# Performance work log

Hardware: AMD Instinct MI355X
Metric: run time of the kernel (lower is better)

Reference implementation:

```python
import jax, jax.numpy as jnp
import numpy as np

H, NH, L, S, B, V = 512, 8, 6, 2048, 2, 32000
DH = H // NH
EPS = 1e-5


def posenc(h, s):
    pos = jnp.arange(s, dtype=jnp.float32)[:, None]
    div = jnp.power(10000.0, jnp.arange(0, h, 2, dtype=jnp.float32) / h)
    pe = jnp.zeros((s, h), dtype=jnp.float32)
    pe = pe.at[:, 0::2].set(jnp.sin(pos / div))
    pe = pe.at[:, 1::2].set(jnp.cos(pos / div))
    return pe


def layernorm(x, g, b):
    mu = jnp.mean(x, axis=-1, keepdims=True)
    var = jnp.mean(jnp.square(x - mu), axis=-1, keepdims=True)
    return (x - mu) * jax.lax.rsqrt(var + EPS) * g + b


def setup_inputs() -> dict:
    key = jax.random.key(0)
    ks = jax.random.split(key, 16)
    sc = 0.02
    return {
        "src": jax.random.randint(ks[0], (B, S), 0, V),
        "mask": jnp.ones((B, 1, 1, S), dtype=jnp.int32),
        "emb": jax.random.normal(ks[1], (V, H), jnp.float32) * sc,
        "Wq": jax.random.normal(ks[2], (L, H, H), jnp.float32) * sc,
        "bq": jnp.zeros((L, H), jnp.float32),
        "Wk": jax.random.normal(ks[3], (L, H, H), jnp.float32) * sc,
        "bk": jnp.zeros((L, H), jnp.float32),
        "Wv": jax.random.normal(ks[4], (L, H, H), jnp.float32) * sc,
        "bv": jnp.zeros((L, H), jnp.float32),
        "Wo": jax.random.normal(ks[5], (L, H, H), jnp.float32) * sc,
        "bo": jnp.zeros((L, H), jnp.float32),
        "gamma": jnp.ones((L, H), jnp.float32),
        "beta": jnp.zeros((L, H), jnp.float32),
        "W1": jax.random.normal(ks[6], (L, H, 4 * H), jnp.float32) * sc,
        "b1": jnp.zeros((L, 4 * H), jnp.float32),
        "W2": jax.random.normal(ks[7], (L, 4 * H, H), jnp.float32) * sc,
        "b2": jnp.zeros((L, H), jnp.float32),
    }


def reference(src, mask, emb, Wq, bq, Wk, bk, Wv, bv, Wo, bo, gamma, beta, W1, b1, W2, b2):
    x = emb[src] + posenc(H, S)[None, :, :]  # [B,S,H]
    for i in range(L):
        q = (x @ Wq[i] + bq[i]).reshape(B, S, NH, DH).transpose(0, 2, 1, 3)
        k = (x @ Wk[i] + bk[i]).reshape(B, S, NH, DH).transpose(0, 2, 1, 3)
        v = (x @ Wv[i] + bv[i]).reshape(B, S, NH, DH).transpose(0, 2, 1, 3)
        scores = jnp.einsum("bhqd,bhkd->bhqk", q, k) / jnp.sqrt(jnp.float32(DH))
        scores = jnp.where(mask == 0, jnp.float32(-1e20), scores)
        attn = jax.nn.softmax(scores, axis=-1)
        av = jnp.einsum("bhqk,bhkd->bhqd", attn, v)
        attn_out = av.transpose(0, 2, 1, 3).reshape(B, S, H) @ Wo[i] + bo[i]
        # NOTE: same LayerNorm params applied to both sublayers (as in source)
        res = x + layernorm(attn_out, gamma[i], beta[i])
        ffn = jax.nn.relu(res @ W1[i] + b1[i]) @ W2[i] + b2[i]
        x = res + layernorm(ffn, gamma[i], beta[i])
    return x
```

## Files before the change

kernel.cpp:

```cpp
#include <hip/hip_runtime.h>
#include <math.h>

#define HDIM 512
#define NHEAD 8
#define NLAYER 6
#define SEQ 2048
#define BATCH 2
#define DHEAD 64
#define TOKENS (BATCH*SEQ)
#define FFND (4*HDIM)
#define QSTR 1536

typedef unsigned short u16;
typedef __attribute__((ext_vector_type(8))) short short8;
typedef __attribute__((ext_vector_type(4))) float f32x4;

__device__ __forceinline__ u16 f2b(float f) {
  unsigned u = __float_as_uint(f);
  u += 0x7FFFu + ((u >> 16) & 1u);
  return (u16)(u >> 16);
}

__device__ __forceinline__ unsigned cvtpk_bf16(float lo, float hi) {
  unsigned r;
  asm("v_cvt_pk_bf16_f32 %0, %1, %2" : "=v"(r) : "v"(lo), "v"(hi));
  return r;
}

__device__ __forceinline__ void gload_lds16(const u16* g, u16* l) {
  __builtin_amdgcn_global_load_lds((const __attribute__((address_space(1))) void*)g,
                                   (__attribute__((address_space(3))) void*)l, 16, 0, 0);
}

__global__ void embed_pe(const int* __restrict__ src, const float* __restrict__ emb,
                         float* __restrict__ X, u16* __restrict__ Xb) {
  int tok = blockIdx.x;
  int lane = threadIdx.x;
  int s = tok & (SEQ - 1);
  int c0 = lane * 8;
  const float* e = emb + (long)src[tok] * HDIM + c0;
  float v[8];
#pragma unroll
  for (int j = 0; j < 8; j++) {
    int c = c0 + j;
    float arg = (float)s * exp2f(-(float)(c & ~1) * 0.02595256917f);
    v[j] = e[j] + ((c & 1) ? cosf(arg) : sinf(arg));
  }
  float* xp = X + (long)tok * HDIM + c0;
#pragma unroll
  for (int j = 0; j < 8; j++) xp[j] = v[j];
  u16 hb[8];
#pragma unroll
  for (int j = 0; j < 8; j++) hb[j] = f2b(v[j]);
  uint4 pk;
  pk.x = hb[0] | ((unsigned)hb[1] << 16);
  pk.y = hb[2] | ((unsigned)hb[3] << 16);
  pk.z = hb[4] | ((unsigned)hb[5] << 16);
  pk.w = hb[6] | ((unsigned)hb[7] << 16);
  *(uint4*)(Xb + (long)tok * HDIM + c0) = pk;
}

__global__ __launch_bounds__(256) void prep_weights(
    const float* __restrict__ Wq, const float* __restrict__ Wk, const float* __restrict__ Wv,
    const float* __restrict__ Wo, const float* __restrict__ W1, const float* __restrict__ W2,
    const float* __restrict__ bq, const float* __restrict__ bk, const float* __restrict__ bv,
    u16* __restrict__ Wqkvt, u16* __restrict__ Wot, u16* __restrict__ W1t, u16* __restrict__ W2t,
    float* __restrict__ bqkv) {
  int t = blockIdx.x;
  int tid = threadIdx.x;
  if (t == 768) {
    for (int i = tid; i < 1536; i += 256)
      bqkv[i] = (i < 512) ? bq[i] : (i < 1024) ? bk[i - 512] : bv[i - 1024];
    return;
  }
  const float* src; u16* dst; int K, N, kt, nt; long drow0 = 0;
  if (t < 192)      { int m = t / 64, r = t % 64; src = (m==0)?Wq:(m==1)?Wk:Wv; dst = Wqkvt; drow0 = (long)m*512; K=512;  N=512;  kt=r/8;  nt=r%8; }
  else if (t < 256) { int r = t - 192; src = Wo; dst = Wot; K=512;  N=512;  kt=r/8;  nt=r%8; }
  else if (t < 512) { int r = t - 256; src = W1; dst = W1t; K=512;  N=2048; kt=r/32; nt=r%32; }
  else              { int r = t - 512; src = W2; dst = W2t; K=2048; N=512;  kt=r/8;  nt=r%8; }
  __shared__ __align__(16) u16 Lt[64 * 72];
  int kl = tid >> 2;
#pragma unroll
  for (int rr = 0; rr < 4; rr++) {
    int cl = (tid & 3) * 4 + rr * 16;
    float4 v = *(const float4*)(src + (long)(kt * 64 + kl) * N + nt * 64 + cl);
    Lt[(cl + 0) * 72 + kl] = f2b(v.x);
    Lt[(cl + 1) * 72 + kl] = f2b(v.y);
    Lt[(cl + 2) * 72 + kl] = f2b(v.z);
    Lt[(cl + 3) * 72 + kl] = f2b(v.w);
  }
  __syncthreads();
  int nl = tid >> 2;
  int kc = (tid & 3) * 16;
  u16* dp = dst + (drow0 + nt * 64 + nl) * (long)K + kt * 64 + kc;
  *(uint4*)dp       = *(const uint4*)&Lt[nl * 72 + kc];
  *(uint4*)(dp + 8) = *(const uint4*)&Lt[nl * 72 + kc + 8];
}

__global__ __launch_bounds__(256) void vtranspose(const u16* __restrict__ QKV,
                                                  u16* __restrict__ Vtb) {
  __shared__ __align__(16) u16 Lt[64 * 72];
  int tid = threadIdx.x;
  int bh = blockIdx.y, b = bh >> 3, h = bh & 7;
  int s0 = blockIdx.x * 64;
  const u16* vsrc = QKV + (long)(b * SEQ + s0) * QSTR + 1024 + h * DHEAD;
  int key = tid >> 2, dc = (tid & 3) * 16;
  const u16* vp = vsrc + (long)key * QSTR + dc;
  uint4 v0 = *(const uint4*)vp;
  uint4 v1 = *(const uint4*)(vp + 8);
  unsigned vr[8] = { v0.x, v0.y, v0.z, v0.w, v1.x, v1.y, v1.z, v1.w };
#pragma unroll
  for (int j = 0; j < 8; j++) {
    Lt[(dc + 2 * j) * 72 + key]     = (u16)vr[j];
    Lt[(dc + 2 * j + 1) * 72 + key] = (u16)(vr[j] >> 16);
  }
  __syncthreads();
  int d = tid >> 2, kc = (tid & 3) * 16;
  u16* dst = Vtb + ((long)bh * DHEAD + d) * SEQ + s0 + kc;
  *(uint4*)dst       = *(const uint4*)&Lt[d * 72 + kc];
  *(uint4*)(dst + 8) = *(const uint4*)&Lt[d * 72 + kc + 8];
}

template <int BN, int KSPLIT, bool RELU, bool WF32, bool WB16>
__global__ __launch_bounds__(256) void gemm_tn(const u16* __restrict__ A,
                                               const u16* __restrict__ Bt,
                                               const float* __restrict__ bias,
                                               float* __restrict__ Cf,
                                               u16* __restrict__ Cb,
                                               int M, int N, int K) {
  constexpr int NF = BN / 32;
  __shared__ __align__(16) u16 As[2][128 * 32];
  __shared__ __align__(16) u16 Bs[2][BN * 32];
  int tid = threadIdx.x;
  int wave = tid >> 6, lane = tid & 63;
  int ln = lane & 15, hi = lane >> 4;
  int wm = wave >> 1, wn = wave & 1;
  int m0 = blockIdx.y * 128, n0 = blockIdx.x * BN;
  int z = (KSPLIT > 1) ? blockIdx.z : 0;
  int Ks = K / KSPLIT;
  const u16* Ab = A + z * Ks;
  const u16* Bb = Bt + z * Ks;

  f32x4 acc[4][NF] = {};

  int srow = lane >> 2;
  int skc  = (lane & 3) * 8;

  auto issue = [&](int kt, int buf) {
    int k0 = kt * 32;
#pragma unroll
    for (int j = 0; j < 2; j++) {
      int row = (wave * 2 + j) * 16 + srow;
      gload_lds16(Ab + (long)(m0 + row) * K + k0 + skc, &As[buf][row * 32 + skc]);
    }
#pragma unroll
    for (int j = 0; j < BN / 64; j++) {
      int row = (wave * (BN / 64) + j) * 16 + srow;
      gload_lds16(Bb + (long)(n0 + row) * K + k0 + skc, &Bs[buf][row * 32 + skc]);
    }
  };

  int NT = Ks / 32;
  issue(0, 0);
  __syncthreads();
  for (int kt = 0; kt < NT; kt++) {
    int buf = kt & 1;
    if (kt + 1 < NT) issue(kt + 1, buf ^ 1);
    short8 af[4], bf[NF];
#pragma unroll
    for (int mt = 0; mt < 4; mt++)
      af[mt] = *(const short8*)&As[buf][(wm * 64 + mt * 16 + ln) * 32 + 8 * hi];
#pragma unroll
    for (int nt = 0; nt < NF; nt++)
      bf[nt] = *(const short8*)&Bs[buf][(wn * (BN / 2) + nt * 16 + ln) * 32 + 8 * hi];
#pragma unroll
    for (int mt = 0; mt < 4; mt++)
#pragma unroll
      for (int nt = 0; nt < NF; nt++)
        acc[mt][nt] = __builtin_amdgcn_mfma_f32_16x16x32_bf16(af[mt], bf[nt], acc[mt][nt], 0, 0, 0);
    __syncthreads();
  }

  float* Cz = WF32 ? (Cf + (long)z * M * N) : nullptr;
#pragma unroll
  for (int mt = 0; mt < 4; mt++)
#pragma unroll
    for (int nt = 0; nt < NF; nt++)
#pragma unroll
      for (int r = 0; r < 4; r++) {
        int row = m0 + wm * 64 + mt * 16 + hi * 4 + r;
        int col = n0 + wn * (BN / 2) + nt * 16 + ln;
        float v = acc[mt][nt][r];
        if (KSPLIT == 1 || z == 0) v += bias[col];
        if (RELU) v = fmaxf(v, 0.0f);
        if (WF32) Cz[(long)row * N + col] = v;
        if (WB16) Cb[(long)row * N + col] = f2b(v);
      }
}

__global__ __launch_bounds__(256) void attention(const u16* __restrict__ QKV,
                                                 const u16* __restrict__ Vtb,
                                                 const int* __restrict__ mask,
                                                 u16* __restrict__ Og) {
  __shared__ __align__(16) u16 Ks[2][64 * 64];
  __shared__ __align__(16) u16 Vs[2][64 * 64];
  int tid = threadIdx.x, w = tid >> 6, lane = tid & 63;
  int ln = lane & 15, hi = lane >> 4;
  int h0 = hi & 1, h1 = hi >> 1, ln7 = ln & 7;
  int bh = blockIdx.y, b = bh >> 3, h = bh & 7;
  int q0 = blockIdx.x * 64 + w * 16;
  const u16* qbase = QKV + (long)b * SEQ * QSTR + h * DHEAD;
  const u16* kbase = qbase + 512;
  const u16* vtbase = Vtb + (long)bh * DHEAD * SEQ;
  const int* mrow = mask + b * SEQ;

  short8 qf[2];
#pragma unroll
  for (int ks = 0; ks < 2; ks++)
    qf[ks] = *(const short8*)(qbase + (long)(q0 + ln) * QSTR + ks * 32 + 8 * hi);

  int sr0 = tid >> 3, sc = tid & 7;
  const u16 *kp0, *kp1, *vp0, *vp1;
  {
    int r1 = sr0 + 32;
    int key0 = (sr0 & 7) | ((sr0 & 0x18) << 1) | ((sr0 & 0x20) >> 2);
    int key1 = (r1 & 7) | ((r1 & 0x18) << 1) | ((r1 & 0x20) >> 2);
    kp0 = kbase + (long)key0 * QSTR + (sc ^ (sr0 & 7)) * 8;
    kp1 = kbase + (long)key1 * QSTR + (sc ^ (r1 & 7)) * 8;
    vp0 = vtbase + (long)sr0 * SEQ + (sc ^ (sr0 & 7)) * 8;
    vp1 = vtbase + (long)r1 * SEQ + (sc ^ (r1 & 7)) * 8;
  }
  int d0 = sr0 * 64 + sc * 8, d1 = d0 + 2048;

  auto issue = [&](int t, int buf) {
    long ko = (long)t * (64 * QSTR);
    int vo = t * 64;
    gload_lds16(kp0 + ko, &Ks[buf][d0]);
    gload_lds16(kp1 + ko, &Ks[buf][d1]);
    gload_lds16(vp0 + vo, &Vs[buf][d0]);
    gload_lds16(vp1 + vo, &Vs[buf][d1]);
  };

  f32x4 o[4] = {};
  float lsum = 0.0f;
  const int NT = SEQ / 64;
  issue(0, 0);
  __syncthreads();
  for (int t = 0; t < NT; t++) {
    int buf = t & 1;
    const int* mbase = mrow + t * 64 + 16 * h1 + 4 * h0;
    int4 mv[4];
    mv[0] = *(const int4*)(mbase);
    mv[1] = *(const int4*)(mbase + 32);
    mv[2] = *(const int4*)(mbase + 8);
    mv[3] = *(const int4*)(mbase + 40);
    if (t + 1 < NT) issue(t + 1, buf ^ 1);

    f32x4 s[4] = {};
#pragma unroll
    for (int ks = 0; ks < 2; ks++)
#pragma unroll
      for (int kb = 0; kb < 4; kb++) {
        short8 kf = *(const short8*)&Ks[buf][(kb * 16 + ln) * 64 + (((ks << 2) + hi) ^ ln7) * 8];
        s[kb] = __builtin_amdgcn_mfma_f32_16x16x32_bf16(kf, qf[ks], s[kb], 0, 0, 0);
      }

    unsigned D[4][2];
#pragma unroll
    for (int kb = 0; kb < 4; kb++) {
      float p[4];
#pragma unroll
      for (int r = 0; r < 4; r++) {
        float pv = __expf(s[kb][r] * 0.125f);
        int m = (&mv[kb].x)[r];
        pv = m ? pv : 0.0f;
        lsum += pv;
        p[r] = pv;
      }
      D[kb][0] = cvtpk_bf16(p[0], p[1]);
      D[kb][1] = cvtpk_bf16(p[2], p[3]);
    }

    short8 pb[2];
#pragma unroll
    for (int ks = 0; ks < 2; ks++) {
      unsigned own0 = h0 ? D[2 + ks][0] : D[ks][0];
      unsigned own1 = h0 ? D[2 + ks][1] : D[ks][1];
      unsigned snd0 = h0 ? D[ks][0] : D[2 + ks][0];
      unsigned snd1 = h0 ? D[ks][1] : D[2 + ks][1];
      unsigned rc0 = (unsigned)__shfl_xor((int)snd0, 16);
      unsigned rc1 = (unsigned)__shfl_xor((int)snd1, 16);
      union { unsigned u[4]; short8 v; } pu;
      pu.u[0] = h0 ? rc0 : own0;
      pu.u[1] = h0 ? rc1 : own1;
      pu.u[2] = h0 ? own0 : rc0;
      pu.u[3] = h0 ? own1 : rc1;
      pb[ks] = pu.v;
    }

#pragma unroll
    for (int ks = 0; ks < 2; ks++)
#pragma unroll
      for (int mb = 0; mb < 4; mb++) {
        short8 vf = *(const short8*)&Vs[buf][(mb * 16 + ln) * 64 + (((ks << 2) + hi) ^ ln7) * 8];
        o[mb] = __builtin_amdgcn_mfma_f32_16x16x32_bf16(vf, pb[ks], o[mb], 0, 0, 0);
      }
    __syncthreads();
  }

  lsum += __shfl_xor(lsum, 16);
  lsum += __shfl_xor(lsum, 32);
  float rl = 1.0f / lsum;

  u16* Ot = &Ks[0][0] + w * 1024;
#pragma unroll
  for (int mb = 0; mb < 4; mb++) {
    *(unsigned*)&Ot[ln * 64 + mb * 16 + hi * 4 + 0] = cvtpk_bf16(o[mb][0] * rl, o[mb][1] * rl);
    *(unsigned*)&Ot[ln * 64 + mb * 16 + hi * 4 + 2] = cvtpk_bf16(o[mb][2] * rl, o[mb][3] * rl);
  }
  __syncthreads();
  u16* obase = Og + (long)b * SEQ * HDIM + h * DHEAD;
#pragma unroll
  for (int pass = 0; pass < 2; pass++) {
    int row = (lane >> 3) + 8 * pass;
    int c = lane & 7;
    uint4 val = *(const uint4*)&Ot[row * 64 + c * 8];
    *(uint4*)(obase + (long)(q0 + row) * HDIM + c * 8) = val;
  }
}

__global__ __launch_bounds__(256) void ln_residual(const float* __restrict__ Xin,
                                                   const float* __restrict__ T0,
                                                   const float* __restrict__ T1,
                                                   const float* __restrict__ gamma,
                                                   const float* __restrict__ beta,
                                                   float* __restrict__ Xout,
                                                   u16* __restrict__ Xb) {
  int tid = threadIdx.x, w = tid >> 6, lane = tid & 63;
  int row = blockIdx.x * 4 + w;
  const float* t0 = T0 + (long)row * HDIM;
  const float* t1 = T1 + (long)row * HDIM;
  int c0 = lane * 8;
  float v[8];
  {
    float4 a0 = *(const float4*)(t0 + c0);
    float4 b0 = *(const float4*)(t0 + c0 + 4);
    float4 a1 = *(const float4*)(t1 + c0);
    float4 b1 = *(const float4*)(t1 + c0 + 4);
    v[0] = a0.x + a1.x; v[1] = a0.y + a1.y; v[2] = a0.z + a1.z; v[3] = a0.w + a1.w;
    v[4] = b0.x + b1.x; v[5] = b0.y + b1.y; v[6] = b0.z + b1.z; v[7] = b0.w + b1.w;
  }
  float sum = 0.0f;
#pragma unroll
  for (int j = 0; j < 8; j++) sum += v[j];
#pragma unroll
  for (int off = 32; off; off >>= 1) sum += __shfl_xor(sum, off);
  float mu = sum * (1.0f / HDIM);
  float sq = 0.0f;
#pragma unroll
  for (int j = 0; j < 8; j++) { float d = v[j] - mu; sq += d * d; }
#pragma unroll
  for (int off = 32; off; off >>= 1) sq += __shfl_xor(sq, off);
  float rs = rsqrtf(sq * (1.0f / HDIM) + 1e-5f);
  const float* xin = Xin + (long)row * HDIM + c0;
  float* xout = Xout + (long)row * HDIM + c0;
  u16 hb[8];
#pragma unroll
  for (int j = 0; j < 8; j++) {
    int c = c0 + j;
    float y = xin[j] + (v[j] - mu) * rs * gamma[c] + beta[c];
    xout[j] = y;
    hb[j] = f2b(y);
  }
  uint4 pk;
  pk.x = hb[0] | ((unsigned)hb[1] << 16);
  pk.y = hb[2] | ((unsigned)hb[3] << 16);
  pk.z = hb[4] | ((unsigned)hb[5] << 16);
  pk.w = hb[6] | ((unsigned)hb[7] << 16);
  *(uint4*)(Xb + (long)row * HDIM + c0) = pk;
}

extern "C" void kernel_launch(void* const* d_in, const int* in_sizes, int n_in,
                              void* d_out, int out_size, void* d_ws, size_t ws_size,
                              hipStream_t stream) {
  const int*   src   = (const int*)d_in[0];
  const int*   mask  = (const int*)d_in[1];
  const float* emb   = (const float*)d_in[2];
  const float* Wq    = (const float*)d_in[3];
  const float* bq    = (const float*)d_in[4];
  const float* Wk    = (const float*)d_in[5];
  const float* bk    = (const float*)d_in[6];
  const float* Wv    = (const float*)d_in[7];
  const float* bv    = (const float*)d_in[8];
  const float* Wo    = (const float*)d_in[9];
  const float* bo    = (const float*)d_in[10];
  const float* gamma = (const float*)d_in[11];
  const float* beta  = (const float*)d_in[12];
  const float* W1    = (const float*)d_in[13];
  const float* b1    = (const float*)d_in[14];
  const float* W2    = (const float*)d_in[15];
  const float* b2    = (const float*)d_in[16];

  char* ws = (char*)d_ws;
  float* X     = (float*)(ws);
  u16*   Xb    = (u16*)(ws + (8ll << 20));
  u16*   QKVb  = (u16*)(ws + (12ll << 20));
  u16*   Mb    = (u16*)(ws + (12ll << 20));
  u16*   AVb   = (u16*)(ws + (24ll << 20));
  float* T     = (float*)(ws + (28ll << 20));
  u16*   Wqkvt = (u16*)(ws + (44ll << 20));
  u16*   Wot   = (u16*)(ws + (45ll << 20) + (512ll << 10));
  u16*   W1t   = (u16*)(ws + (46ll << 20));
  u16*   W2t   = (u16*)(ws + (48ll << 20));
  float* bqkv  = (float*)(ws + (50ll << 20));
  u16*   Vtb   = (u16*)(ws + (51ll << 20));
  float* T1    = T + (long)TOKENS * HDIM;

  embed_pe<<<dim3(TOKENS), dim3(64), 0, stream>>>(src, emb, X, Xb);

  for (int i = 0; i < NLAYER; i++) {
    long wo = (long)i * HDIM * HDIM;
    prep_weights<<<dim3(769), 256, 0, stream>>>(
        Wq + wo, Wk + wo, Wv + wo, Wo + wo,
        W1 + (long)i * HDIM * FFND, W2 + (long)i * FFND * HDIM,
        bq + i * HDIM, bk + i * HDIM, bv + i * HDIM,
        Wqkvt, Wot, W1t, W2t, bqkv);

    gemm_tn<128, 1, false, false, true><<<dim3(QSTR / 128, TOKENS / 128), 256, 0, stream>>>(
        Xb, Wqkvt, bqkv, nullptr, QKVb, TOKENS, QSTR, HDIM);

    vtranspose<<<dim3(SEQ / 64, BATCH * NHEAD), 256, 0, stream>>>(QKVb, Vtb);

    attention<<<dim3(SEQ / 64, BATCH * NHEAD), 256, 0, stream>>>(QKVb, Vtb, mask, AVb);

    gemm_tn<64, 2, false, true, false><<<dim3(HDIM / 64, TOKENS / 128, 2), 256, 0, stream>>>(
        AVb, Wot, bo + i * HDIM, T, nullptr, TOKENS, HDIM, HDIM);

    ln_residual<<<dim3(TOKENS / 4), 256, 0, stream>>>(X, T, T1, gamma + i * HDIM,
                                                      beta + i * HDIM, X, Xb);

    gemm_tn<128, 1, true, false, true><<<dim3(FFND / 128, TOKENS / 128), 256, 0, stream>>>(
        Xb, W1t, b1 + (long)i * FFND, nullptr, Mb, TOKENS, FFND, HDIM);

    gemm_tn<64, 2, false, true, false><<<dim3(HDIM / 64, TOKENS / 128, 2), 256, 0, stream>>>(
        Mb, W2t, b2 + i * HDIM, T, nullptr, TOKENS, HDIM, FFND);

    ln_residual<<<dim3(TOKENS / 4), 256, 0, stream>>>(X, T, T1, gamma + i * HDIM,
                                                      beta + i * HDIM, X, Xb);
  }

  hipMemcpyAsync(d_out, X, (size_t)TOKENS * HDIM * sizeof(float),
                 hipMemcpyDeviceToDevice, stream);
}
```

Before: 1.070 ms.

## Bitpack attention mask, deepen K/V prefetch, and remap attention blocks

Packs the int mask into one 64-bit word per 64-key tile in a one-time kernel and stages those words in LDS. The attention loop no longer does per-tile global int4 mask loads and takes a branch-free exp path when a tile is fully unmasked. The K/V pipeline now keeps two tiles in flight using explicit vmcnt waits and raw s_barriers in place of __syncthreads. The grid is flattened and remapped so consecutive blocks spread across heads, which is meant to improve placement across XCDs. The cost is more fragile hand-written synchronisation, with a risk of LDS races if the wait counts are wrong.

Measured after the change: 1.012 ms. 1.06x faster.

```diff
diff --git a/kernel.cpp b/kernel.cpp
--- a/kernel.cpp
+++ b/kernel.cpp
@@ -12,6 +12,7 @@
 #define QSTR 1536
 
 typedef unsigned short u16;
+typedef unsigned long long u64;
 typedef __attribute__((ext_vector_type(8))) short short8;
 typedef __attribute__((ext_vector_type(4))) float f32x4;
 
@@ -58,6 +59,16 @@
   pk.z = hb[4] | ((unsigned)hb[5] << 16);
   pk.w = hb[6] | ((unsigned)hb[7] << 16);
   *(uint4*)(Xb + (long)tok * HDIM + c0) = pk;
+}
+
+__global__ void maskprep(const int* __restrict__ mask, u64* __restrict__ mb) {
+  int t = threadIdx.x;
+  int b = t >> 5, tile = t & 31;
+  const int* m = mask + b * SEQ + tile * 64;
+  u64 w = 0;
+#pragma unroll
+  for (int j = 0; j < 64; j++) w |= (u64)(m[j] != 0) << j;
+  mb[t] = w;
 }
 
 __global__ __launch_bounds__(256) void prep_weights(
@@ -200,24 +211,30 @@
 
 __global__ __launch_bounds__(256) void attention(const u16* __restrict__ QKV,
                                                  const u16* __restrict__ Vtb,
-                                                 const int* __restrict__ mask,
+                                                 const u64* __restrict__ maskb,
                                                  u16* __restrict__ Og) {
   __shared__ __align__(16) u16 Ks[2][64 * 64];
   __shared__ __align__(16) u16 Vs[2][64 * 64];
+  __shared__ u64 Msk[SEQ / 64];
   int tid = threadIdx.x, w = tid >> 6, lane = tid & 63;
   int ln = lane & 15, hi = lane >> 4;
   int h0 = hi & 1, h1 = hi >> 1, ln7 = ln & 7;
-  int bh = blockIdx.y, b = bh >> 3, h = bh & 7;
-  int q0 = blockIdx.x * 64 + w * 16;
+  int lin = blockIdx.x;
+  int lid = (lin & 7) * 64 + (lin >> 3);
+  int bh = lid >> 5, qt = lid & 31;
+  int b = bh >> 3, h = bh & 7;
+  int q0 = qt * 64 + w * 16;
   const u16* qbase = QKV + (long)b * SEQ * QSTR + h * DHEAD;
   const u16* kbase = qbase + 512;
   const u16* vtbase = Vtb + (long)bh * DHEAD * SEQ;
-  const int* mrow = mask + b * SEQ;
 
   short8 qf[2];
 #pragma unroll
   for (int ks = 0; ks < 2; ks++)
     qf[ks] = *(const short8*)(qbase + (long)(q0 + ln) * QSTR + ks * 32 + 8 * hi);
+
+  u64 mw0 = 0;
+  if (tid < SEQ / 64) mw0 = maskb[b * (SEQ / 64) + tid];
 
   int sr0 = tid >> 3, sc = tid & 7;
   const u16 *kp0, *kp1, *vp0, *vp1;
@@ -244,17 +261,18 @@
   f32x4 o[4] = {};
   float lsum = 0.0f;
   const int NT = SEQ / 64;
+
   issue(0, 0);
-  __syncthreads();
+  issue(1, 1);
+  if (tid < SEQ / 64) Msk[tid] = mw0;
+  asm volatile("s_waitcnt vmcnt(4)" ::: "memory");
+  __builtin_amdgcn_sched_barrier(0);
+  __builtin_amdgcn_s_barrier();
+  __builtin_amdgcn_sched_barrier(0);
+
   for (int t = 0; t < NT; t++) {
     int buf = t & 1;
-    const int* mbase = mrow + t * 64 + 16 * h1 + 4 * h0;
-    int4 mv[4];
-    mv[0] = *(const int4*)(mbase);
-    mv[1] = *(const int4*)(mbase + 32);
-    mv[2] = *(const int4*)(mbase + 8);
-    mv[3] = *(const int4*)(mbase + 40);
-    if (t + 1 < NT) issue(t + 1, buf ^ 1);
+    u64 mw = Msk[t];
 
     f32x4 s[4] = {};
 #pragma unroll
@@ -266,19 +284,37 @@
       }
 
     unsigned D[4][2];
-#pragma unroll
-    for (int kb = 0; kb < 4; kb++) {
-      float p[4];
-#pragma unroll
-      for (int r = 0; r < 4; r++) {
-        float pv = __expf(s[kb][r] * 0.125f);
-        int m = (&mv[kb].x)[r];
-        pv = m ? pv : 0.0f;
-        lsum += pv;
-        p[r] = pv;
+    if (mw == 0xFFFFFFFFFFFFFFFFull) {
+#pragma unroll
+      for (int kb = 0; kb < 4; kb++) {
+        float p[4];
+#pragma unroll
+        for (int r = 0; r < 4; r++) {
+          float pv = __expf(s[kb][r] * 0.125f);
+          lsum += pv;
+          p[r] = pv;
+        }
+        D[kb][0] = cvtpk_bf16(p[0], p[1]);
+        D[kb][1] = cvtpk_bf16(p[2], p[3]);
       }
-      D[kb][0] = cvtpk_bf16(p[0], p[1]);
-      D[kb][1] = cvtpk_bf16(p[2], p[3]);
+    } else {
+      unsigned shb = h1 * 16 + h0 * 4;
+      u64 mws = mw >> shb;
+      unsigned nib[4] = { (unsigned)mws & 0xFu, (unsigned)(mws >> 32) & 0xFu,
+                          (unsigned)(mws >> 8) & 0xFu, (unsigned)(mws >> 40) & 0xFu };
+#pragma unroll
+      for (int kb = 0; kb < 4; kb++) {
+        float p[4];
+#pragma unroll
+        for (int r = 0; r < 4; r++) {
+          float pv = __expf(s[kb][r] * 0.125f);
+          pv = ((nib[kb] >> r) & 1u) ? pv : 0.0f;
+          lsum += pv;
+          p[r] = pv;
+        }
+        D[kb][0] = cvtpk_bf16(p[0], p[1]);
+        D[kb][1] = cvtpk_bf16(p[2], p[3]);
+      }
     }
 
     short8 pb[2];
@@ -305,7 +341,20 @@
         short8 vf = *(const short8*)&Vs[buf][(mb * 16 + ln) * 64 + (((ks << 2) + hi) ^ ln7) * 8];
         o[mb] = __builtin_amdgcn_mfma_f32_16x16x32_bf16(vf, pb[ks], o[mb], 0, 0, 0);
       }
-    __syncthreads();
+
+    asm volatile("s_waitcnt lgkmcnt(0)" ::: "memory");
+    __builtin_amdgcn_sched_barrier(0);
+    __builtin_amdgcn_s_barrier();
+    __builtin_amdgcn_sched_barrier(0);
+    if (t + 2 < NT) {
+      issue(t + 2, buf);
+      asm volatile("s_waitcnt vmcnt(4)" ::: "memory");
+    } else {
+      asm volatile("s_waitcnt vmcnt(0)" ::: "memory");
+    }
+    __builtin_amdgcn_sched_barrier(0);
+    __builtin_amdgcn_s_barrier();
+    __builtin_amdgcn_sched_barrier(0);
   }
 
   lsum += __shfl_xor(lsum, 16);
@@ -318,7 +367,8 @@
     *(unsigned*)&Ot[ln * 64 + mb * 16 + hi * 4 + 0] = cvtpk_bf16(o[mb][0] * rl, o[mb][1] * rl);
     *(unsigned*)&Ot[ln * 64 + mb * 16 + hi * 4 + 2] = cvtpk_bf16(o[mb][2] * rl, o[mb][3] * rl);
   }
-  __syncthreads();
+  asm volatile("s_waitcnt lgkmcnt(0)" ::: "memory");
+  __builtin_amdgcn_s_barrier();
   u16* obase = Og + (long)b * SEQ * HDIM + h * DHEAD;
 #pragma unroll
   for (int pass = 0; pass < 2; pass++) {
@@ -414,9 +464,11 @@
   u16*   W2t   = (u16*)(ws + (48ll << 20));
   float* bqkv  = (float*)(ws + (50ll << 20));
   u16*   Vtb   = (u16*)(ws + (51ll << 20));
+  u64*   maskbits = (u64*)(ws + (55ll << 20));
   float* T1    = T + (long)TOKENS * HDIM;
 
   embed_pe<<<dim3(TOKENS), dim3(64), 0, stream>>>(src, emb, X, Xb);
+  maskprep<<<dim3(1), dim3(64), 0, stream>>>(mask, maskbits);
 
   for (int i = 0; i < NLAYER; i++) {
     long wo = (long)i * HDIM * HDIM;
@@ -431,7 +483,7 @@
 
     vtranspose<<<dim3(SEQ / 64, BATCH * NHEAD), 256, 0, stream>>>(QKVb, Vtb);
 
-    attention<<<dim3(SEQ / 64, BATCH * NHEAD), 256, 0, stream>>>(QKVb, Vtb, mask, AVb);
+    attention<<<dim3(512), 256, 0, stream>>>(QKVb, Vtb, maskbits, AVb);
 
     gemm_tn<64, 2, false, true, false><<<dim3(HDIM / 64, TOKENS / 128, 2), 256, 0, stream>>>(
         AVb, Wot, bo + i * HDIM, T, nullptr, TOKENS, HDIM, HDIM);
```
